# Kernel optimization log

Hardware: AMD Instinct MI355X
Metric: run time of the kernel (lower is better)

## Reference

```python
import jax, jax.numpy as jnp
import numpy as np

D = 1024        # hidden_size = input_size = output_size
E = 8           # num_experts
K = 2           # top-k
TEMP = 1.0      # router temperature


def setup_inputs() -> dict:
    key = jax.random.key(0)
    ks = jax.random.split(key, 7)
    s = 0.02
    x = jax.random.normal(ks[0], (4, 2048, D), dtype=jnp.float32)
    w_router = jax.random.normal(ks[1], (D, E), dtype=jnp.float32) * s
    w1 = jax.random.normal(ks[2], (E, D, D), dtype=jnp.float32) * s
    b1 = jnp.zeros((E, D), dtype=jnp.float32)
    w2 = jax.random.normal(ks[3], (E, D, D), dtype=jnp.float32) * s
    b2 = jnp.zeros((E, D), dtype=jnp.float32)
    return {"x": x, "w_router": w_router, "w1": w1, "b1": b1, "w2": w2, "b2": b2}


def reference(x, w_router, w1, b1, w2, b2):
    B, S, _ = x.shape
    # Router: temperature-scaled logits, softmax, top-k
    logits = jnp.einsum('bsd,de->bse', x, w_router) / TEMP          # [B,S,E]
    probs = jax.nn.softmax(logits, axis=-1)
    top_k_probs, top_k_idx = jax.lax.top_k(probs, K)                # [B,S,K]
    xt = x.reshape(-1, D)                                           # [T,D]
    idx = top_k_idx.reshape(-1, K)                                  # [T,K]
    pk = top_k_probs.reshape(-1, K)                                 # [T,K]
    # Dense expert eval: every expert on every token (faithful to source)
    h = jax.nn.gelu(jnp.einsum('td,edh->eth', xt, w1) + b1[:, None, :])
    expert_out = jnp.einsum('eth,ehd->etd', h, w2) + b2[:, None, :]  # [E,T,D]
    expert_out = jnp.transpose(expert_out, (1, 0, 2))                # [T,E,D]
    # Gather selected experts and combine with routing probs
    sel = jnp.take_along_axis(expert_out, idx[:, :, None], axis=1)   # [T,K,D]
    combined = jnp.sum(sel * pk[:, :, None], axis=1)                 # [T,D]
    return combined.reshape(B, S, D), logits
```

## Files before the change

### kernel.cpp

```cpp
#include <hip/hip_runtime.h>
#include <hip/hip_bf16.h>

#define DH 1024
#define NE 8
#define NT 8192
#define NTK 16384

typedef __bf16 bf16x8 __attribute__((ext_vector_type(8)));
typedef float f32x4 __attribute__((ext_vector_type(4)));
typedef unsigned short u16;
typedef u16 u16x8 __attribute__((ext_vector_type(8)));
typedef u16 u16x4 __attribute__((ext_vector_type(4)));

__device__ __forceinline__ u16 f2bf(float f) {
  union { float f; unsigned u; } v; v.f = f;
  return (u16)((v.u + 0x7fffu + ((v.u >> 16) & 1u)) >> 16);
}
__device__ __forceinline__ float bf2f(u16 h) {
  union { unsigned u; float f; } v; v.u = ((unsigned)h) << 16;
  return v.f;
}
__device__ __forceinline__ float gelu_tanh(float v) {
  float y = 0.7978845608028654f * (v + 0.044715f * v * v * v);
  float t = 1.f - 2.f / (1.f + __expf(2.f * y));
  return 0.5f * v * (1.f + t);
}

__global__ __launch_bounds__(256) void prep_transpose(
    const float* __restrict__ w1, const float* __restrict__ w2,
    u16* __restrict__ w1t, u16* __restrict__ w2t) {
  __shared__ float tile[64][65];
  int z = blockIdx.z;
  const float* src = (z < NE) ? (w1 + (size_t)z * DH * DH) : (w2 + (size_t)(z - NE) * DH * DH);
  u16* dst = (z < NE) ? (w1t + (size_t)z * DH * DH) : (w2t + (size_t)(z - NE) * DH * DH);
  int d0 = blockIdx.y * 64, n0 = blockIdx.x * 64;
  int tid = threadIdx.x;
  int c = tid & 63, r = tid >> 6;
#pragma unroll
  for (int it = 0; it < 16; ++it) {
    int rr = r + it * 4;
    tile[rr][c] = src[(size_t)(d0 + rr) * DH + n0 + c];
  }
  __syncthreads();
#pragma unroll
  for (int it = 0; it < 16; ++it) {
    int rr = r + it * 4;
    dst[(size_t)(n0 + rr) * DH + d0 + c] = f2bf(tile[c][rr]);
  }
}

__global__ __launch_bounds__(256) void convert_x(const float* __restrict__ x,
                                                 u16* __restrict__ xb) {
  size_t gid = (size_t)blockIdx.x * 256 + threadIdx.x;
  const float4* p = (const float4*)(x + gid * 8);
  float4 f0 = p[0], f1 = p[1];
  u16x8 o;
  o[0] = f2bf(f0.x); o[1] = f2bf(f0.y); o[2] = f2bf(f0.z); o[3] = f2bf(f0.w);
  o[4] = f2bf(f1.x); o[5] = f2bf(f1.y); o[6] = f2bf(f1.z); o[7] = f2bf(f1.w);
  *(u16x8*)(xb + gid * 8) = o;
}

__global__ __launch_bounds__(256) void router_kernel(
    const float* __restrict__ x, const float* __restrict__ wr,
    float* __restrict__ logits_out, int* __restrict__ tkidx,
    float* __restrict__ tkp, int* __restrict__ counts) {
  __shared__ float wsh[NE][DH + 8];
  __shared__ int hist[NE];
  int tid = threadIdx.x;
  for (int i = tid; i < DH * NE; i += 256) {
    int d = i >> 3, e = i & 7;
    wsh[e][d] = wr[i];
  }
  if (tid < NE) hist[tid] = 0;
  __syncthreads();

  int lane = tid & 63;
  int wv = tid >> 6;
  int t0 = blockIdx.x * 32 + wv * 8;
#pragma unroll 1
  for (int i = 0; i < 8; ++i) {
    int t = t0 + i;
    const float4* xp = (const float4*)(x + (size_t)t * DH);
    float a[8] = {0.f, 0.f, 0.f, 0.f, 0.f, 0.f, 0.f, 0.f};
#pragma unroll
    for (int it = 0; it < 4; ++it) {
      float4 xv = xp[it * 64 + lane];
      int d0 = (it * 64 + lane) * 4;
#pragma unroll
      for (int e = 0; e < 8; ++e) {
        float4 w4 = *(const float4*)&wsh[e][d0];
        a[e] += xv.x * w4.x + xv.y * w4.y + xv.z * w4.z + xv.w * w4.w;
      }
    }
#pragma unroll
    for (int off = 32; off; off >>= 1) {
#pragma unroll
      for (int e = 0; e < 8; ++e) a[e] += __shfl_xor(a[e], off, 64);
    }
    if (lane < 8) logits_out[(size_t)t * NE + lane] = a[lane];
    if (lane == 0) {
      float m1 = a[0]; int i1 = 0;
#pragma unroll
      for (int e = 1; e < 8; ++e) if (a[e] > m1) { m1 = a[e]; i1 = e; }
      float m2 = -3.4e38f; int i2 = 0;
#pragma unroll
      for (int e = 0; e < 8; ++e) if (e != i1 && a[e] > m2) { m2 = a[e]; i2 = e; }
      float den = 0.f;
#pragma unroll
      for (int e = 0; e < 8; ++e) den += expf(a[e] - m1);
      tkidx[2 * t] = i1; tkidx[2 * t + 1] = i2;
      tkp[2 * t] = 1.0f / den;
      tkp[2 * t + 1] = expf(m2 - m1) / den;
      atomicAdd(&hist[i1], 1);
      atomicAdd(&hist[i2], 1);
    }
  }
  __syncthreads();
  if (tid < NE) atomicAdd(&counts[tid], hist[tid]);
}

__global__ void offsets_kernel(const int* __restrict__ counts,
                               int* __restrict__ offs, int* __restrict__ cur) {
  if (threadIdx.x == 0) {
    int s = 0;
    for (int e = 0; e < NE; ++e) { offs[e] = s; s += counts[e]; cur[e] = 0; }
    offs[NE] = s;
  }
}

__global__ __launch_bounds__(1024) void scatter_kernel(
    const int* __restrict__ tkidx, const float* __restrict__ tkp,
    const int* __restrict__ offs, int* __restrict__ cur,
    int* __restrict__ rows, int* __restrict__ posof, float* __restrict__ pp) {
  __shared__ int h[NE];
  __shared__ int base[NE];
  int tid = threadIdx.x;
  int gid = blockIdx.x * 1024 + tid;
  if (tid < NE) h[tid] = 0;
  __syncthreads();
  int e = tkidx[gid];
  int myrank = atomicAdd(&h[e], 1);
  __syncthreads();
  if (tid < NE) base[tid] = atomicAdd(&cur[tid], h[tid]);
  __syncthreads();
  int pos = offs[e] + base[e] + myrank;
  rows[pos] = gid >> 1;
  posof[gid] = pos;
  pp[pos] = tkp[gid];
}

template <int GELU>
__global__ __launch_bounds__(256) void gemm_kernel(
    const u16* __restrict__ A, const u16* __restrict__ W,
    const float* __restrict__ bias, const int* __restrict__ counts,
    const int* __restrict__ offs, const int* __restrict__ rows,
    u16* __restrict__ outb) {
  int e = blockIdx.z;
  int cnt = counts[e];
  int m0 = blockIdx.y * 128;
  if (m0 >= cnt) return;
  int n0 = blockIdx.x * 128;
  int seg = offs[e];

  __shared__ __attribute__((aligned(16))) u16 As[128][72];
  __shared__ __attribute__((aligned(16))) u16 Bs[128][72];

  int tid = threadIdx.x;
  int arow = tid >> 1;
  int kh = (tid & 1) * 32;

  int gi = m0 + arow;
  int clamp = gi < cnt ? gi : cnt - 1;
  const u16* aptr;
  if (GELU) {
    aptr = A + (size_t)rows[seg + clamp] * DH + kh;
  } else {
    aptr = A + (size_t)(seg + clamp) * DH + kh;
  }
  const u16* bptr = W + (size_t)e * DH * DH + (size_t)(n0 + arow) * DH + kh;

  int lane = tid & 63;
  int wv = tid >> 6;
  int wrr = (wv >> 1) * 64, wcc = (wv & 1) * 64;
  int lr = lane & 15;
  int kg8 = (lane >> 4) * 8;

  f32x4 acc[4][4] = {};

  for (int k0 = 0; k0 < DH; k0 += 64) {
    u16x8 av[4], bv[4];
#pragma unroll
    for (int j = 0; j < 4; ++j) {
      av[j] = *(const u16x8*)(aptr + k0 + j * 8);
      bv[j] = *(const u16x8*)(bptr + k0 + j * 8);
    }
    __syncthreads();
#pragma unroll
    for (int j = 0; j < 4; ++j) {
      *(u16x8*)&As[arow][kh + j * 8] = av[j];
      *(u16x8*)&Bs[arow][kh + j * 8] = bv[j];
    }
    __syncthreads();
#pragma unroll
    for (int ks = 0; ks < 64; ks += 32) {
      bf16x8 af[4], bfv[4];
#pragma unroll
      for (int m = 0; m < 4; ++m) af[m] = *(const bf16x8*)&As[wrr + m * 16 + lr][ks + kg8];
#pragma unroll
      for (int n = 0; n < 4; ++n) bfv[n] = *(const bf16x8*)&Bs[wcc + n * 16 + lr][ks + kg8];
#pragma unroll
      for (int m = 0; m < 4; ++m)
#pragma unroll
        for (int n = 0; n < 4; ++n)
          acc[m][n] = __builtin_amdgcn_mfma_f32_16x16x32_bf16(af[m], bfv[n], acc[m][n], 0, 0, 0);
    }
  }

  int r4 = (lane >> 4) * 4;
  const float* be = bias + (size_t)e * DH;
#pragma unroll
  for (int m = 0; m < 4; ++m) {
#pragma unroll
    for (int n = 0; n < 4; ++n) {
      int col = n0 + wcc + n * 16 + lr;
      float bvv = be[col];
#pragma unroll
      for (int j = 0; j < 4; ++j) {
        int gr = m0 + wrr + m * 16 + r4 + j;
        if (gr < cnt) {
          float v = acc[m][n][j] + bvv;
          if (GELU) v = gelu_tanh(v);
          outb[(size_t)(seg + gr) * DH + col] = f2bf(v);
        }
      }
    }
  }
}

__global__ __launch_bounds__(256) void combine_kernel(
    const u16* __restrict__ eo, const float* __restrict__ tkp,
    const int* __restrict__ posof, float* __restrict__ out) {
  int gid = blockIdx.x * 256 + threadIdx.x;
  int t = gid >> 8;
  int n = (gid & 255) * 4;
  float p0 = tkp[2 * t], p1 = tkp[2 * t + 1];
  int q0 = posof[2 * t], q1 = posof[2 * t + 1];
  u16x4 a = *(const u16x4*)(eo + (size_t)q0 * DH + n);
  u16x4 b = *(const u16x4*)(eo + (size_t)q1 * DH + n);
  float4 o;
  o.x = p0 * bf2f(a[0]) + p1 * bf2f(b[0]);
  o.y = p0 * bf2f(a[1]) + p1 * bf2f(b[1]);
  o.z = p0 * bf2f(a[2]) + p1 * bf2f(b[2]);
  o.w = p0 * bf2f(a[3]) + p1 * bf2f(b[3]);
  *(float4*)(out + (size_t)t * DH + n) = o;
}

extern "C" void kernel_launch(void* const* d_in, const int* in_sizes, int n_in,
                              void* d_out, int out_size, void* d_ws, size_t ws_size,
                              hipStream_t stream) {
  const float* x = (const float*)d_in[0];
  const float* w_router = (const float*)d_in[1];
  const float* w1 = (const float*)d_in[2];
  const float* b1 = (const float*)d_in[3];
  const float* w2 = (const float*)d_in[4];
  const float* b2 = (const float*)d_in[5];
  float* out = (float*)d_out;
  float* logits = out + (size_t)NT * DH;

  char* ws = (char*)d_ws;
  size_t off = 0;
  auto alloc = [&](size_t bytes) -> void* {
    void* p = ws + off;
    off = (off + bytes + 255) & ~(size_t)255;
    return p;
  };
  int* ctrl = (int*)alloc(256);
  int* counts = ctrl;
  int* cur = ctrl + 8;
  int* offs = ctrl + 16;
  int* tkidx = (int*)alloc((size_t)NTK * 4);
  float* tkp = (float*)alloc((size_t)NTK * 4);
  int* rows = (int*)alloc((size_t)NTK * 4);
  int* posof = (int*)alloc((size_t)NTK * 4);
  float* pp = (float*)alloc((size_t)NTK * 4);
  u16* w1t = (u16*)alloc((size_t)NE * DH * DH * 2);
  u16* w2t = (u16*)alloc((size_t)NE * DH * DH * 2);
  u16* hbuf = (u16*)alloc((size_t)NTK * DH * 2);
  u16* eo = (u16*)alloc((size_t)NTK * DH * 2);
  u16* xb = eo;

  hipMemsetAsync(ctrl, 0, 256, stream);

  prep_transpose<<<dim3(16, 16, 16), 256, 0, stream>>>(w1, w2, w1t, w2t);
  convert_x<<<(NT * DH / 8) / 256, 256, 0, stream>>>(x, xb);
  router_kernel<<<NT / 32, 256, 0, stream>>>(x, w_router, logits, tkidx, tkp, counts);
  offsets_kernel<<<1, 64, 0, stream>>>(counts, offs, cur);
  scatter_kernel<<<NTK / 1024, 1024, 0, stream>>>(tkidx, tkp, offs, cur, rows, posof, pp);
  gemm_kernel<1><<<dim3(8, 128, 8), 256, 0, stream>>>(xb, w1t, b1, counts, offs, rows, hbuf);
  gemm_kernel<0><<<dim3(8, 128, 8), 256, 0, stream>>>(hbuf, w2t, b2, counts, offs, rows, eo);
  combine_kernel<<<NT, 256, 0, stream>>>(eo, tkp, posof, out);
}
```

Baseline: 221.2 us.

## Use direct global-to-LDS loads and compact tile map for grouped expert GEMMs

Replaces the register-staged global→LDS copy in the grouped GEMM with global_load_lds direct 16-byte transfers into an unpadded LDS layout, saving VGPRs and a store pass. It also builds a compact (expert, m-tile) map in the offsets kernel, so the GEMM grid launches 136 row tiles instead of 8×128 mostly-empty blocks. The unpadded LDS rows of 64 bf16 may cause bank conflicts on the MFMA fragment reads. There is still no double buffering, so loads and compute do not overlap.

```diff
diff --git a/kernel.cpp b/kernel.cpp
--- a/kernel.cpp
+++ b/kernel.cpp
@@ -5,6 +5,9 @@
 #define NE 8
 #define NT 8192
 #define NTK 16384
+#define BM 128
+#define BN 128
+#define BK 64
 
 typedef __bf16 bf16x8 __attribute__((ext_vector_type(8)));
 typedef float f32x4 __attribute__((ext_vector_type(4)));
@@ -24,6 +27,12 @@
   float y = 0.7978845608028654f * (v + 0.044715f * v * v * v);
   float t = 1.f - 2.f / (1.f + __expf(2.f * y));
   return 0.5f * v * (1.f + t);
+}
+
+__device__ __forceinline__ void gload_lds16(const u16* g, u16* l) {
+  __builtin_amdgcn_global_load_lds(
+      (const __attribute__((address_space(1))) void*)g,
+      (__attribute__((address_space(3))) void*)l, 16, 0, 0);
 }
 
 __global__ __launch_bounds__(256) void prep_transpose(
@@ -120,11 +129,18 @@
 }
 
 __global__ void offsets_kernel(const int* __restrict__ counts,
-                               int* __restrict__ offs, int* __restrict__ cur) {
+                               int* __restrict__ offs, int* __restrict__ cur,
+                               int* __restrict__ tmap) {
   if (threadIdx.x == 0) {
     int s = 0;
     for (int e = 0; e < NE; ++e) { offs[e] = s; s += counts[e]; cur[e] = 0; }
     offs[NE] = s;
+    int t = 0;
+    for (int e = 0; e < NE; ++e)
+      for (int m0 = 0; m0 < counts[e]; m0 += BM) {
+        tmap[1 + 2 * t] = e; tmap[2 + 2 * t] = m0; ++t;
+      }
+    tmap[0] = t;
   }
 }
 
@@ -154,66 +170,68 @@
     const u16* __restrict__ A, const u16* __restrict__ W,
     const float* __restrict__ bias, const int* __restrict__ counts,
     const int* __restrict__ offs, const int* __restrict__ rows,
-    u16* __restrict__ outb) {
-  int e = blockIdx.z;
+    const int* __restrict__ tmap, u16* __restrict__ outb) {
+  int ty = blockIdx.y;
+  if (ty >= tmap[0]) return;
+  int e = tmap[1 + 2 * ty];
+  int m0 = tmap[2 + 2 * ty];
   int cnt = counts[e];
-  int m0 = blockIdx.y * 128;
-  if (m0 >= cnt) return;
-  int n0 = blockIdx.x * 128;
   int seg = offs[e];
-
-  __shared__ __attribute__((aligned(16))) u16 As[128][72];
-  __shared__ __attribute__((aligned(16))) u16 Bs[128][72];
+  int n0 = blockIdx.x * BN;
+
+  __shared__ __attribute__((aligned(16))) u16 As[BM * BK];
+  __shared__ __attribute__((aligned(16))) u16 Bs[BN * BK];
 
   int tid = threadIdx.x;
-  int arow = tid >> 1;
-  int kh = (tid & 1) * 32;
-
-  int gi = m0 + arow;
-  int clamp = gi < cnt ? gi : cnt - 1;
-  const u16* aptr;
-  if (GELU) {
-    aptr = A + (size_t)rows[seg + clamp] * DH + kh;
-  } else {
-    aptr = A + (size_t)(seg + clamp) * DH + kh;
-  }
-  const u16* bptr = W + (size_t)e * DH * DH + (size_t)(n0 + arow) * DH + kh;
-
   int lane = tid & 63;
   int wv = tid >> 6;
-  int wrr = (wv >> 1) * 64, wcc = (wv & 1) * 64;
+  int lrow = lane >> 3;
+  int lk8 = (lane & 7) * 8;
+
+  const u16* aSrc[4];
+  const u16* bSrc[4];
+  const u16* bBase = W + (size_t)e * DH * DH + lk8;
+#pragma unroll
+  for (int i = 0; i < 4; ++i) {
+    int gi = m0 + i * 32 + wv * 8 + lrow;
+    int cl = gi < cnt ? gi : cnt - 1;
+    int arow = GELU ? rows[seg + cl] : (seg + cl);
+    aSrc[i] = A + (size_t)arow * DH + lk8;
+    int gn = n0 + i * 32 + wv * 8 + lrow;
+    bSrc[i] = bBase + (size_t)gn * DH;
+  }
+  u16* aDst = As + (size_t)(wv * 8) * BK;
+  u16* bDst = Bs + (size_t)(wv * 8) * BK;
+
   int lr = lane & 15;
   int kg8 = (lane >> 4) * 8;
+  int wrr = (wv >> 1) * 64, wcc = (wv & 1) * 64;
 
   f32x4 acc[4][4] = {};
 
-  for (int k0 = 0; k0 < DH; k0 += 64) {
-    u16x8 av[4], bv[4];
-#pragma unroll
-    for (int j = 0; j < 4; ++j) {
-      av[j] = *(const u16x8*)(aptr + k0 + j * 8);
-      bv[j] = *(const u16x8*)(bptr + k0 + j * 8);
+  for (int k0 = 0; k0 < DH; k0 += BK) {
+#pragma unroll
+    for (int i = 0; i < 4; ++i) {
+      gload_lds16(aSrc[i] + k0, aDst + i * 32 * BK);
+      gload_lds16(bSrc[i] + k0, bDst + i * 32 * BK);
     }
     __syncthreads();
 #pragma unroll
-    for (int j = 0; j < 4; ++j) {
-      *(u16x8*)&As[arow][kh + j * 8] = av[j];
-      *(u16x8*)&Bs[arow][kh + j * 8] = bv[j];
-    }
-    __syncthreads();
-#pragma unroll
-    for (int ks = 0; ks < 64; ks += 32) {
+    for (int ks = 0; ks < BK; ks += 32) {
       bf16x8 af[4], bfv[4];
 #pragma unroll
-      for (int m = 0; m < 4; ++m) af[m] = *(const bf16x8*)&As[wrr + m * 16 + lr][ks + kg8];
-#pragma unroll
-      for (int n = 0; n < 4; ++n) bfv[n] = *(const bf16x8*)&Bs[wcc + n * 16 + lr][ks + kg8];
+      for (int m = 0; m < 4; ++m)
+        af[m] = *(const bf16x8*)&As[(size_t)(wrr + m * 16 + lr) * BK + ks + kg8];
+#pragma unroll
+      for (int n = 0; n < 4; ++n)
+        bfv[n] = *(const bf16x8*)&Bs[(size_t)(wcc + n * 16 + lr) * BK + ks + kg8];
 #pragma unroll
       for (int m = 0; m < 4; ++m)
 #pragma unroll
         for (int n = 0; n < 4; ++n)
           acc[m][n] = __builtin_amdgcn_mfma_f32_16x16x32_bf16(af[m], bfv[n], acc[m][n], 0, 0, 0);
     }
+    __syncthreads();
   }
 
   int r4 = (lane >> 4) * 4;
@@ -278,6 +296,7 @@
   int* counts = ctrl;
   int* cur = ctrl + 8;
   int* offs = ctrl + 16;
+  int* tmap = (int*)alloc(2048);
   int* tkidx = (int*)alloc((size_t)NTK * 4);
   float* tkp = (float*)alloc((size_t)NTK * 4);
   int* rows = (int*)alloc((size_t)NTK * 4);
@@ -294,9 +313,9 @@
   prep_transpose<<<dim3(16, 16, 16), 256, 0, stream>>>(w1, w2, w1t, w2t);
   convert_x<<<(NT * DH / 8) / 256, 256, 0, stream>>>(x, xb);
   router_kernel<<<NT / 32, 256, 0, stream>>>(x, w_router, logits, tkidx, tkp, counts);
-  offsets_kernel<<<1, 64, 0, stream>>>(counts, offs, cur);
+  offsets_kernel<<<1, 64, 0, stream>>>(counts, offs, cur, tmap);
   scatter_kernel<<<NTK / 1024, 1024, 0, stream>>>(tkidx, tkp, offs, cur, rows, posof, pp);
-  gemm_kernel<1><<<dim3(8, 128, 8), 256, 0, stream>>>(xb, w1t, b1, counts, offs, rows, hbuf);
-  gemm_kernel<0><<<dim3(8, 128, 8), 256, 0, stream>>>(hbuf, w2t, b2, counts, offs, rows, eo);
+  gemm_kernel<1><<<dim3(8, 136, 1), 256, 0, stream>>>(xb, w1t, b1, counts, offs, rows, tmap, hbuf);
+  gemm_kernel<0><<<dim3(8, 136, 1), 256, 0, stream>>>(hbuf, w2t, b2, counts, offs, rows, tmap, eo);
   combine_kernel<<<NT, 256, 0, stream>>>(eo, tkp, posof, out);
 }
```

Measured after the change: 243.4 us. 1.1x slower.
